# Performance work log

Hardware: AMD Instinct MI355X
Metric: run time of the kernel (lower is better)

The kernel has to match this reference:

```python
import jax, jax.numpy as jnp
import numpy as np

TOKENS, D_IN = 8192, 1024
E, D_OUT = 8, 1024
H = 2 * D_OUT  # Expert hidden = 2 * num_outputs


def setup_inputs() -> dict:
    key = jax.random.key(0)
    ks = jax.random.split(key, 4)
    s_in = 1.0 / np.sqrt(D_IN)
    s_h = 1.0 / np.sqrt(H)
    return {
        "x": jax.random.normal(ks[0], (TOKENS, D_IN), dtype=jnp.float32),
        "W1": jax.random.normal(ks[1], (E, D_IN, H), dtype=jnp.float32) * s_in,
        "b1": jnp.zeros((E, H), dtype=jnp.float32),
        "W2": jax.random.normal(ks[2], (E, H, D_OUT), dtype=jnp.float32) * s_h,
        "b2": jnp.zeros((E, D_OUT), dtype=jnp.float32),
        "Wg": jax.random.normal(ks[3], (D_IN, E), dtype=jnp.float32) * s_in,
        "bg": jnp.zeros((E,), dtype=jnp.float32),
    }


def reference(x, W1, b1, W2, b2, Wg, bg):
    # Gating: softmax over experts. gates: [N, E]
    gates = jax.nn.softmax(x @ Wg + bg, axis=-1)
    # All experts run densely: batched GEMM over expert axis.
    h = jax.nn.relu(jnp.einsum('nd,edh->neh', x, W1) + b1)       # [N, E, H]
    expert_out = jnp.einsum('neh,ehf->nef', h, W2) + b2          # [N, E, D_OUT]
    # Gate-weighted sum over experts (fused stack*gate->sum).
    return jnp.einsum('nef,ne->nf', expert_out, gates)            # [N, D_OUT]
```

## Files before the change

### kernel.cpp

```cpp
#include <hip/hip_runtime.h>
#include <stdint.h>

#define TOKENS 8192
#define D_IN   1024
#define NEXP   8
#define D_OUT  1024
#define HDIM   2048

typedef __bf16 bf16x8 __attribute__((ext_vector_type(8)));
typedef __bf16 bf16x4 __attribute__((ext_vector_type(4)));
typedef float  f32x4  __attribute__((ext_vector_type(4)));

__device__ __forceinline__ void gload16(const void* g, void* l) {
  __builtin_amdgcn_global_load_lds(
      (const __attribute__((address_space(1))) void*)g,
      (__attribute__((address_space(3))) void*)l,
      16, 0, 0);
}

template <int N>
__device__ __forceinline__ void waitv() {
  if constexpr (N == 0)      asm volatile("s_waitcnt vmcnt(0)" ::: "memory");
  else if constexpr (N == 1) asm volatile("s_waitcnt vmcnt(1)" ::: "memory");
  else if constexpr (N == 2) asm volatile("s_waitcnt vmcnt(2)" ::: "memory");
  else if constexpr (N == 3) asm volatile("s_waitcnt vmcnt(3)" ::: "memory");
  else if constexpr (N == 4) asm volatile("s_waitcnt vmcnt(4)" ::: "memory");
  else static_assert(N <= 4, "unsupported vmcnt");
}

__global__ void gate_kernel(const float* __restrict__ x,
                            const float* __restrict__ Wg,
                            const float* __restrict__ bg,
                            float* __restrict__ gates) {
  const int lane = threadIdx.x & 63;
  const int n = blockIdx.x * 4 + (threadIdx.x >> 6);
  float acc[NEXP];
#pragma unroll
  for (int e = 0; e < NEXP; ++e) acc[e] = 0.f;
  const float* xr = x + (size_t)n * D_IN;
  for (int d = lane; d < D_IN; d += 64) {
    float xv = xr[d];
    const float* wr = Wg + d * NEXP;
#pragma unroll
    for (int e = 0; e < NEXP; ++e) acc[e] += xv * wr[e];
  }
#pragma unroll
  for (int e = 0; e < NEXP; ++e) {
    float v = acc[e];
#pragma unroll
    for (int off = 32; off > 0; off >>= 1) v += __shfl_down(v, off);
    acc[e] = v;
  }
  if (lane == 0) {
    float mx = -1e30f;
#pragma unroll
    for (int e = 0; e < NEXP; ++e) { acc[e] += bg[e]; mx = fmaxf(mx, acc[e]); }
    float s = 0.f;
#pragma unroll
    for (int e = 0; e < NEXP; ++e) { acc[e] = expf(acc[e] - mx); s += acc[e]; }
    float inv = 1.f / s;
#pragma unroll
    for (int e = 0; e < NEXP; ++e) gates[n * NEXP + e] = acc[e] * inv;
  }
}

__global__ void cvt_x_kernel(const float* __restrict__ x, __bf16* __restrict__ xb) {
  const int stride = gridDim.x * blockDim.x;
  const int total4 = TOKENS * D_IN / 4;
  for (int i = blockIdx.x * blockDim.x + threadIdx.x; i < total4; i += stride) {
    float4 v = ((const float4*)x)[i];
    bf16x4 o;
    o[0] = (__bf16)v.x; o[1] = (__bf16)v.y; o[2] = (__bf16)v.z; o[3] = (__bf16)v.w;
    ((bf16x4*)xb)[i] = o;
  }
}

__global__ void transpose_cvt_kernel(const float* __restrict__ W,
                                     __bf16* __restrict__ Wt,
                                     int K, int N, int EPG) {
  __shared__ float tile[32][33];
  const int e = blockIdx.z;
  const int ldo = EPG * K;
  const float* Win = W + (size_t)e * K * N;
  __bf16* Wout = Wt + (size_t)(e / EPG) * N * ldo + (size_t)(e % EPG) * K;
  const int n0 = blockIdx.x * 32;
  const int k0 = blockIdx.y * 32;
  const int tx = threadIdx.x & 31;
  const int ty = threadIdx.x >> 5;
#pragma unroll
  for (int r = ty; r < 32; r += 8)
    tile[r][tx] = Win[(size_t)(k0 + r) * N + n0 + tx];
  __syncthreads();
#pragma unroll
  for (int r = ty; r < 32; r += 8)
    Wout[(size_t)(n0 + r) * ldo + k0 + tx] = (__bf16)tile[tx][r];
}

__global__ void merge_kernel(float* __restrict__ out,
                             const float* __restrict__ acc1,
                             const float* __restrict__ gates,
                             const float* __restrict__ b2,
                             int use_acc1) {
  const int idx = blockIdx.x * 256 + threadIdx.x;
  const int n = idx >> 8;
  const int fb = idx & 255;
  float4 o = ((const float4*)out)[idx];
  if (use_acc1) {
    float4 a = ((const float4*)acc1)[idx];
    o.x += a.x; o.y += a.y; o.z += a.z; o.w += a.w;
  }
  const float* g = gates + (size_t)n * NEXP;
#pragma unroll
  for (int e = 0; e < NEXP; ++e) {
    const float ge = g[e];
    float4 b = ((const float4*)(b2 + (size_t)e * D_OUT))[fb];
    o.x += ge * b.x; o.y += ge * b.y; o.z += ge * b.z; o.w += ge * b.w;
  }
  ((float4*)out)[idx] = o;
}

template <int BM, int BN, int WM, int WN, int EPI>
__global__ __launch_bounds__(512, 2)
void moe_gemm(const __bf16* __restrict__ A, size_t AZ,
              const __bf16* __restrict__ B, size_t BZ,
              const float* __restrict__ b1g,
              const float* __restrict__ gates,
              int e0,
              __bf16* __restrict__ Hout, size_t HZ, int OCZ, int ldo,
              float* __restrict__ F0, float* __restrict__ F1,
              int first, int M, int N, int K) {
  constexpr int RM = BM / WM, RN = BN / WN;
  constexpr int FM = RM / 16, FN = RN / 16;
  constexpr int HM = FM / 2,  HN = FN / 2;
  constexpr int LA = BM / 128;
  constexpr int LB = BN / 128;
  constexpr int AELEM = BM * 64;
  constexpr int SLOT  = (BM + BN) * 64;
  __shared__ alignas(16) __bf16 lds[2 * SLOT];

  const int tid  = threadIdx.x;
  const int lane = tid & 63;
  const int wave = tid >> 6;
  const int wr   = wave / WN;
  const int wc   = wave % WN;
  const int lrow = lane & 15;
  const int khi  = lane >> 4;
  const int sx   = (lrow & 7) << 3;
  const int bz   = blockIdx.z;

  A += (size_t)bz * AZ;
  B += (size_t)bz * BZ;

  const int Gx   = gridDim.x;
  const int nwg  = Gx * gridDim.y;
  const int orig = blockIdx.y * Gx + blockIdx.x;
  const int wgid = (orig & 7) * (nwg >> 3) + (orig >> 3);
  const int bn0  = (wgid % Gx) * BN;
  const int bm0  = (wgid / Gx) * BM;

  const __bf16* srcA[2][LA];
  const __bf16* srcB[2][LB];
#pragma unroll
  for (int q = 0; q < 2; ++q) {
#pragma unroll
    for (int j = 0; j < LA; ++j) {
      int o   = q * (BM * 64) + j * 8192 + tid * 16;
      int row = o >> 7;
      int cb  = (o & 127) ^ ((row & 7) << 4);
      srcA[q][j] = A + (size_t)(bm0 + row) * K + (cb >> 1);
    }
#pragma unroll
    for (int j = 0; j < LB; ++j) {
      int o   = q * (BN * 64) + j * 8192 + tid * 16;
      int row = o >> 7;
      int cb  = (o & 127) ^ ((row & 7) << 4);
      srcB[q][j] = B + (size_t)(bn0 + row) * K + (cb >> 1);
    }
  }

  auto stageA = [&](int kt, int q, int s) {
#pragma unroll
    for (int j = 0; j < LA; ++j)
      gload16(srcA[q][j] + (size_t)kt * 64,
              lds + s * SLOT + q * (BM * 32) + j * 4096 + wave * 512);
  };
  auto stageB = [&](int kt, int q, int s) {
#pragma unroll
    for (int j = 0; j < LB; ++j)
      gload16(srcB[q][j] + (size_t)kt * 64,
              lds + s * SLOT + AELEM + q * (BN * 32) + j * 4096 + wave * 512);
  };

  f32x4 acc[FM][FN];
#pragma unroll
  for (int m = 0; m < FM; ++m)
#pragma unroll
    for (int n = 0; n < FN; ++n) acc[m][n] = f32x4{0.f, 0.f, 0.f, 0.f};

  bf16x8 af[HM][2];
  bf16x8 bf[2][HN][2];

  auto rdA = [&](const __bf16* As, int mq) {
#pragma unroll
    for (int mi = 0; mi < HM; ++mi)
#pragma unroll
      for (int kk = 0; kk < 2; ++kk)
        af[mi][kk] = *(const bf16x8*)
            &As[(size_t)(mq * (BM / 2) + wr * (RM / 2) + mi * 16 + lrow) * 64 +
                ((kk * 32 + khi * 8) ^ sx)];
  };
  auto rdB = [&](const __bf16* Bs, int nq) {
#pragma unroll
    for (int ni = 0; ni < HN; ++ni)
#pragma unroll
      for (int kk = 0; kk < 2; ++kk)
        bf[nq][ni][kk] = *(const bf16x8*)
            &Bs[(size_t)(nq * (BN / 2) + wc * (RN / 2) + ni * 16 + lrow) * 64 +
                ((kk * 32 + khi * 8) ^ sx)];
  };
  auto cluster = [&](int mq, int nq) {
    __builtin_amdgcn_s_setprio(1);
#pragma unroll
    for (int kk = 0; kk < 2; ++kk)
#pragma unroll
      for (int mi = 0; mi < HM; ++mi)
#pragma unroll
        for (int ni = 0; ni < HN; ++ni)
          acc[mq * HM + mi][nq * HN + ni] =
              __builtin_amdgcn_mfma_f32_16x16x32_bf16(
                  af[mi][kk], bf[nq][ni][kk], acc[mq * HM + mi][nq * HN + ni],
                  0, 0, 0);
    __builtin_amdgcn_s_setprio(0);
  };

#define BAR()   asm volatile("s_barrier" ::: "memory")
#define LGKM0() do { asm volatile("s_waitcnt lgkmcnt(0)" ::: "memory"); \
                     __builtin_amdgcn_sched_barrier(0); } while (0)

  const int nk = K >> 6;

  stageA(0, 0, 0); stageB(0, 0, 0); stageA(0, 1, 0); stageB(0, 1, 0);
  waitv<0>();
  BAR();

  for (int t = 0; t < nk; ++t) {
    const int s = t & 1;
    const __bf16* As = lds + s * SLOT;
    const __bf16* Bs = As + AELEM;
    const bool pf = (t + 1 < nk);

    rdA(As, 0); rdB(Bs, 0);
    if (pf) stageA(t + 1, 0, s ^ 1);
    BAR(); LGKM0();
    cluster(0, 0);
    if (pf) waitv<LA>(); else waitv<0>();
    BAR();
    rdB(Bs, 1);
    if (pf) stageB(t + 1, 0, s ^ 1);
    BAR(); LGKM0();
    cluster(0, 1);
    BAR();
    rdA(As, 1);
    if (pf) stageA(t + 1, 1, s ^ 1);
    BAR(); LGKM0();
    cluster(1, 0);
    BAR();
    if (pf) stageB(t + 1, 1, s ^ 1);
    BAR();
    cluster(1, 1);
    if (pf) waitv<LA + LB>(); else waitv<0>();
    BAR();
  }

#undef BAR
#undef LGKM0

  const float* bias = (EPI == 0) ? b1g + (size_t)(e0 + bz) * HDIM : nullptr;
  const int ecol = e0 + bz;
  __bf16* Hp = (EPI == 0) ? Hout + (size_t)bz * HZ + (size_t)bz * OCZ : nullptr;
  float* F = (EPI == 3) ? (bz ? F1 : F0) : nullptr;

#pragma unroll
  for (int m = 0; m < FM; ++m) {
    const int grow0 = bm0 + (m / HM) * (BM / 2) + wr * (RM / 2) +
                      (m % HM) * 16 + khi * 4;
    if constexpr (EPI == 0) {
      float g[4];
#pragma unroll
      for (int r = 0; r < 4; ++r)
        g[r] = gates[(size_t)(grow0 + r) * NEXP + ecol];
#pragma unroll
      for (int n = 0; n < FN; ++n) {
        const int gcol = bn0 + (n / HN) * (BN / 2) + wc * (RN / 2) +
                         (n % HN) * 16 + lrow;
        const float bv = bias[gcol];
        f32x4 a = acc[m][n];
#pragma unroll
        for (int r = 0; r < 4; ++r) {
          float v = a[r] + bv;
          v = v > 0.f ? v : 0.f;
          Hp[(size_t)(grow0 + r) * ldo + gcol] = (__bf16)(v * g[r]);
        }
      }
    } else {
#pragma unroll
      for (int n = 0; n < FN; ++n) {
        const int gcol = bn0 + (n / HN) * (BN / 2) + wc * (RN / 2) +
                         (n % HN) * 16 + lrow;
        f32x4 a = acc[m][n];
#pragma unroll
        for (int r = 0; r < 4; ++r) {
          float* o = F + (size_t)(grow0 + r) * N + gcol;
          if (first) *o = a[r];
          else       *o += a[r];
        }
      }
    }
  }
}

extern "C" void kernel_launch(void* const* d_in, const int* in_sizes, int n_in,
                              void* d_out, int out_size, void* d_ws, size_t ws_size,
                              hipStream_t stream) {
  const float* x  = (const float*)d_in[0];
  const float* W1 = (const float*)d_in[1];
  const float* b1 = (const float*)d_in[2];
  const float* W2 = (const float*)d_in[3];
  const float* b2 = (const float*)d_in[4];
  const float* Wg = (const float*)d_in[5];
  const float* bg = (const float*)d_in[6];
  float* out = (float*)d_out;

  char* w = (char*)d_ws;
  float* gates = (float*)w;   w += (size_t)TOKENS * NEXP * 4;
  __bf16* xb   = (__bf16*)w;  w += (size_t)TOKENS * D_IN * 2;
  __bf16* w1t  = (__bf16*)w;  w += (size_t)NEXP * HDIM * D_IN * 2;
  __bf16* w2c  = (__bf16*)w;  w += (size_t)NEXP * D_OUT * HDIM * 2;
  const size_t base = (size_t)(w - (char*)d_ws);

  const size_t acc_b = (size_t)TOKENS * D_OUT * 4;
  const size_t h1_b  = (size_t)TOKENS * HDIM * 2;
  const int G = (ws_size >= base + acc_b + 4 * h1_b) ? 4
              : (ws_size >= base + acc_b + 2 * h1_b) ? 2 : 1;

  float* acc1 = nullptr;
  if (G > 1) { acc1 = (float*)w; w += acc_b; }
  __bf16* hbuf = (__bf16*)w;

  const size_t WSLICE = (size_t)HDIM * D_IN;

  gate_kernel<<<TOKENS / 4, 256, 0, stream>>>(x, Wg, bg, gates);
  cvt_x_kernel<<<2048, 256, 0, stream>>>(x, xb);
  transpose_cvt_kernel<<<dim3(HDIM / 32, D_IN / 32, NEXP), 256, 0, stream>>>(
      W1, w1t, D_IN, HDIM, 1);
  transpose_cvt_kernel<<<dim3(D_OUT / 32, HDIM / 32, NEXP), 256, 0, stream>>>(
      W2, w2c, HDIM, D_OUT, (G == 4) ? 2 : 1);

  if (G == 4) {
    for (int d = 0; d < 2; ++d) {
      for (int i2 = 0; i2 < 2; ++i2) {
        const int e0 = 4 * d + 2 * i2;
        moe_gemm<256, 256, 2, 4, 0><<<dim3(8, 32, 2), 512, 0, stream>>>(
            xb, 0, w1t + (size_t)e0 * WSLICE, WSLICE, b1, gates, e0,
            hbuf + (size_t)i2 * TOKENS * 4096, 0, HDIM, 2 * HDIM,
            nullptr, nullptr, 0, TOKENS, HDIM, D_IN);
      }
      moe_gemm<256, 256, 2, 4, 3><<<dim3(4, 32, 2), 512, 0, stream>>>(
          hbuf, (size_t)TOKENS * 4096,
          w2c + (size_t)(2 * d) * D_OUT * 4096, (size_t)D_OUT * 4096,
          nullptr, nullptr, 0, nullptr, 0, 0, 2 * HDIM,
          out, acc1, (d == 0) ? 1 : 0, TOKENS, D_OUT, 2 * HDIM);
    }
  } else if (G == 2) {
    for (int d = 0; d < 4; ++d) {
      const int e0 = 2 * d;
      moe_gemm<256, 256, 2, 4, 0><<<dim3(8, 32, 2), 512, 0, stream>>>(
          xb, 0, w1t + (size_t)e0 * WSLICE, WSLICE, b1, gates, e0,
          hbuf, (size_t)TOKENS * HDIM, 0, HDIM,
          nullptr, nullptr, 0, TOKENS, HDIM, D_IN);
      moe_gemm<256, 256, 2, 4, 3><<<dim3(4, 32, 2), 512, 0, stream>>>(
          hbuf, (size_t)TOKENS * HDIM,
          w2c + (size_t)e0 * D_OUT * HDIM, (size_t)D_OUT * HDIM,
          nullptr, nullptr, 0, nullptr, 0, 0, HDIM,
          out, acc1, (d == 0) ? 1 : 0, TOKENS, D_OUT, HDIM);
    }
  } else {
    for (int e = 0; e < NEXP; ++e) {
      moe_gemm<256, 256, 2, 4, 0><<<dim3(8, 32, 1), 512, 0, stream>>>(
          xb, 0, w1t + (size_t)e * WSLICE, 0, b1, gates, e,
          hbuf, 0, 0, HDIM,
          nullptr, nullptr, 0, TOKENS, HDIM, D_IN);
      moe_gemm<256, 128, 4, 2, 3><<<dim3(8, 32, 1), 512, 0, stream>>>(
          hbuf, 0, w2c + (size_t)e * D_OUT * HDIM, 0,
          nullptr, nullptr, 0, nullptr, 0, 0, HDIM,
          out, nullptr, (e == 0) ? 1 : 0, TOKENS, D_OUT, HDIM);
    }
  }

  merge_kernel<<<TOKENS, 256, 0, stream>>>(out, acc1, gates, b2, (G > 1) ? 1 : 0);
}
```

Measured before the change: 694.2 us.

## Single-buffer GEMM LDS with in-place quarter staging and fuse gate with x conversion

The MoE GEMM drops from a double-buffered LDS tile to a single buffer. Each A/B quarter of the next k-tile is streamed in just after its previous contents are consumed, which halves shared-memory use and should help keep two 512-thread workgroups resident per CU. The separate bf16 conversion of x is folded into the gating kernel, so x is read once for both jobs. In exchange, prefetch distance shrinks to within a k-tile and the bf16 store in the gating kernel is a narrow per-lane 2-byte write.

Measured after the change: 655.9 us. 5.5% less time.

```diff
diff --git a/kernel.cpp b/kernel.cpp
--- a/kernel.cpp
+++ b/kernel.cpp
@@ -23,23 +23,26 @@
   if constexpr (N == 0)      asm volatile("s_waitcnt vmcnt(0)" ::: "memory");
   else if constexpr (N == 1) asm volatile("s_waitcnt vmcnt(1)" ::: "memory");
   else if constexpr (N == 2) asm volatile("s_waitcnt vmcnt(2)" ::: "memory");
-  else if constexpr (N == 3) asm volatile("s_waitcnt vmcnt(3)" ::: "memory");
-  else if constexpr (N == 4) asm volatile("s_waitcnt vmcnt(4)" ::: "memory");
-  else static_assert(N <= 4, "unsupported vmcnt");
-}
-
-__global__ void gate_kernel(const float* __restrict__ x,
-                            const float* __restrict__ Wg,
-                            const float* __restrict__ bg,
-                            float* __restrict__ gates) {
+  else static_assert(N <= 2, "unsupported vmcnt");
+}
+
+__global__ void gate_cvt_kernel(const float* __restrict__ x,
+                                const float* __restrict__ Wg,
+                                const float* __restrict__ bg,
+                                float* __restrict__ gates,
+                                __bf16* __restrict__ xb) {
   const int lane = threadIdx.x & 63;
   const int n = blockIdx.x * 4 + (threadIdx.x >> 6);
   float acc[NEXP];
 #pragma unroll
   for (int e = 0; e < NEXP; ++e) acc[e] = 0.f;
   const float* xr = x + (size_t)n * D_IN;
-  for (int d = lane; d < D_IN; d += 64) {
+  __bf16* xo = xb + (size_t)n * D_IN;
+#pragma unroll 4
+  for (int d0 = 0; d0 < D_IN; d0 += 64) {
+    const int d = d0 + lane;
     float xv = xr[d];
+    xo[d] = (__bf16)xv;
     const float* wr = Wg + d * NEXP;
 #pragma unroll
     for (int e = 0; e < NEXP; ++e) acc[e] += xv * wr[e];
@@ -61,17 +64,6 @@
     float inv = 1.f / s;
 #pragma unroll
     for (int e = 0; e < NEXP; ++e) gates[n * NEXP + e] = acc[e] * inv;
-  }
-}
-
-__global__ void cvt_x_kernel(const float* __restrict__ x, __bf16* __restrict__ xb) {
-  const int stride = gridDim.x * blockDim.x;
-  const int total4 = TOKENS * D_IN / 4;
-  for (int i = blockIdx.x * blockDim.x + threadIdx.x; i < total4; i += stride) {
-    float4 v = ((const float4*)x)[i];
-    bf16x4 o;
-    o[0] = (__bf16)v.x; o[1] = (__bf16)v.y; o[2] = (__bf16)v.z; o[3] = (__bf16)v.w;
-    ((bf16x4*)xb)[i] = o;
   }
 }
 
@@ -135,8 +127,7 @@
   constexpr int LA = BM / 128;
   constexpr int LB = BN / 128;
   constexpr int AELEM = BM * 64;
-  constexpr int SLOT  = (BM + BN) * 64;
-  __shared__ alignas(16) __bf16 lds[2 * SLOT];
+  __shared__ alignas(16) __bf16 lds[(BM + BN) * 64];
 
   const int tid  = threadIdx.x;
   const int lane = tid & 63;
@@ -178,17 +169,17 @@
     }
   }
 
-  auto stageA = [&](int kt, int q, int s) {
+  auto stageA = [&](int kt, int q) {
 #pragma unroll
     for (int j = 0; j < LA; ++j)
       gload16(srcA[q][j] + (size_t)kt * 64,
-              lds + s * SLOT + q * (BM * 32) + j * 4096 + wave * 512);
-  };
-  auto stageB = [&](int kt, int q, int s) {
+              lds + q * (BM * 32) + j * 4096 + wave * 512);
+  };
+  auto stageB = [&](int kt, int q) {
 #pragma unroll
     for (int j = 0; j < LB; ++j)
       gload16(srcB[q][j] + (size_t)kt * 64,
-              lds + s * SLOT + AELEM + q * (BN * 32) + j * 4096 + wave * 512);
+              lds + AELEM + q * (BN * 32) + j * 4096 + wave * 512);
   };
 
   f32x4 acc[FM][FN];
@@ -200,23 +191,24 @@
   bf16x8 af[HM][2];
   bf16x8 bf[2][HN][2];
 
-  auto rdA = [&](const __bf16* As, int mq) {
+  auto rdA = [&](int mq) {
 #pragma unroll
     for (int mi = 0; mi < HM; ++mi)
 #pragma unroll
       for (int kk = 0; kk < 2; ++kk)
         af[mi][kk] = *(const bf16x8*)
-            &As[(size_t)(mq * (BM / 2) + wr * (RM / 2) + mi * 16 + lrow) * 64 +
-                ((kk * 32 + khi * 8) ^ sx)];
-  };
-  auto rdB = [&](const __bf16* Bs, int nq) {
+            &lds[(size_t)(mq * (BM / 2) + wr * (RM / 2) + mi * 16 + lrow) * 64 +
+                 ((kk * 32 + khi * 8) ^ sx)];
+  };
+  auto rdB = [&](int nq) {
 #pragma unroll
     for (int ni = 0; ni < HN; ++ni)
 #pragma unroll
       for (int kk = 0; kk < 2; ++kk)
         bf[nq][ni][kk] = *(const bf16x8*)
-            &Bs[(size_t)(nq * (BN / 2) + wc * (RN / 2) + ni * 16 + lrow) * 64 +
-                ((kk * 32 + khi * 8) ^ sx)];
+            &lds[AELEM +
+                 (size_t)(nq * (BN / 2) + wc * (RN / 2) + ni * 16 + lrow) * 64 +
+                 ((kk * 32 + khi * 8) ^ sx)];
   };
   auto cluster = [&](int mq, int nq) {
     __builtin_amdgcn_s_setprio(1);
@@ -239,36 +231,34 @@
 
   const int nk = K >> 6;
 
-  stageA(0, 0, 0); stageB(0, 0, 0); stageA(0, 1, 0); stageB(0, 1, 0);
-  waitv<0>();
+  stageA(0, 0); stageB(0, 0); stageB(0, 1);
+  waitv<LB>();
   BAR();
 
   for (int t = 0; t < nk; ++t) {
-    const int s = t & 1;
-    const __bf16* As = lds + s * SLOT;
-    const __bf16* Bs = As + AELEM;
     const bool pf = (t + 1 < nk);
 
-    rdA(As, 0); rdB(Bs, 0);
-    if (pf) stageA(t + 1, 0, s ^ 1);
+    rdA(0); rdB(0);
+    stageA(t, 1);
     BAR(); LGKM0();
     cluster(0, 0);
-    if (pf) waitv<LA>(); else waitv<0>();
-    BAR();
-    rdB(Bs, 1);
-    if (pf) stageB(t + 1, 0, s ^ 1);
+    waitv<LA>();
+    BAR();
+    rdB(1);
+    if (pf) stageA(t + 1, 0);
     BAR(); LGKM0();
     cluster(0, 1);
-    BAR();
-    rdA(As, 1);
-    if (pf) stageA(t + 1, 1, s ^ 1);
+    if (pf) waitv<LA>(); else waitv<0>();
+    BAR();
+    rdA(1);
+    if (pf) stageB(t + 1, 0);
     BAR(); LGKM0();
     cluster(1, 0);
     BAR();
-    if (pf) stageB(t + 1, 1, s ^ 1);
+    if (pf) stageB(t + 1, 1);
     BAR();
     cluster(1, 1);
-    if (pf) waitv<LA + LB>(); else waitv<0>();
+    if (pf) waitv<LB>();
     BAR();
   }
 
@@ -349,8 +339,7 @@
 
   const size_t WSLICE = (size_t)HDIM * D_IN;
 
-  gate_kernel<<<TOKENS / 4, 256, 0, stream>>>(x, Wg, bg, gates);
-  cvt_x_kernel<<<2048, 256, 0, stream>>>(x, xb);
+  gate_cvt_kernel<<<TOKENS / 4, 256, 0, stream>>>(x, Wg, bg, gates, xb);
   transpose_cvt_kernel<<<dim3(HDIM / 32, D_IN / 32, NEXP), 256, 0, stream>>>(
       W1, w1t, D_IN, HDIM, 1);
   transpose_cvt_kernel<<<dim3(D_OUT / 32, HDIM / 32, NEXP), 256, 0, stream>>>(
```
